# Optimization experiments

Measured on AMD Instinct MI355X. Metric: run time of the kernel, lower is better.

The kernel has to match this reference:

```python
import jax, jax.numpy as jnp
import numpy as np
import functools, math

HEADS = 16


def _query_chunk_attention(query, key, value, precision, key_chunk_size=4096):
    # query: (q_chunk, bh, d); key/value: (kv, bh, d)
    num_kv, num_heads, k_features = key.shape[-3:]
    v_features = value.shape[-1]
    key_chunk_size = min(key_chunk_size, num_kv)
    query = query / jnp.sqrt(k_features)

    @functools.partial(jax.checkpoint, prevent_cse=False)
    def summarize_chunk(query, key, value):
        attn_weights = jnp.einsum("...qhd,...khd->...qhk", query, key, precision=precision)
        max_score = jnp.max(attn_weights, axis=-1, keepdims=True)
        max_score = jax.lax.stop_gradient(max_score)
        exp_weights = jnp.exp(attn_weights - max_score)
        exp_values = jnp.einsum("...vhf,...qhv->...qhf", value, exp_weights, precision=precision)
        max_score = jnp.einsum("...qhk->...qh", max_score)
        return exp_values, exp_weights.sum(axis=-1), max_score

    def chunk_scanner(chunk_idx):
        key_chunk = jax.lax.dynamic_slice(
            key, [chunk_idx, 0, 0], [key_chunk_size, num_heads, k_features])
        value_chunk = jax.lax.dynamic_slice(
            value, [chunk_idx, 0, 0], [key_chunk_size, num_heads, v_features])
        return summarize_chunk(query, key_chunk, value_chunk)

    chunk_values, chunk_weights, chunk_max = jax.lax.map(
        chunk_scanner, xs=jnp.arange(0, num_kv, key_chunk_size))
    # online softmax rescaling across kv chunks
    global_max = jnp.max(chunk_max, axis=0, keepdims=True)
    max_diffs = jnp.exp(chunk_max - global_max)
    chunk_values = chunk_values * jnp.expand_dims(max_diffs, axis=-1)
    chunk_weights = chunk_weights * max_diffs
    all_values = chunk_values.sum(axis=0)
    all_weights = jnp.expand_dims(chunk_weights, -1).sum(axis=0)
    return all_values / all_weights


def jax_memory_efficient_attention(query, key, value,
                                   precision=jax.lax.Precision.HIGHEST,
                                   query_chunk_size=1024, key_chunk_size=4096):
    # query: (q_len, bh, d)
    num_q, num_heads, q_features = query.shape[-3:]

    def chunk_scanner(chunk_idx, _):
        query_chunk = jax.lax.dynamic_slice(
            query, [chunk_idx, 0, 0],
            [min(query_chunk_size, num_q), num_heads, q_features])
        return (chunk_idx + query_chunk_size,
                _query_chunk_attention(query_chunk, key, value, precision, key_chunk_size))

    _, res = jax.lax.scan(chunk_scanner, 0, xs=None,
                          length=math.ceil(num_q / query_chunk_size))
    return jnp.concatenate(res, axis=-3)


def _reshape_heads_to_batch_dim(tensor, heads):
    b, s, d = tensor.shape
    t = tensor.reshape(b, s, heads, d // heads).transpose(0, 2, 1, 3)
    return t.reshape(b * heads, s, d // heads)


def _attention_fwd(query, key, value):
    heads = HEADS
    q = _reshape_heads_to_batch_dim(query, heads).transpose(1, 0, 2)  # (s, b*h, dh)
    k = _reshape_heads_to_batch_dim(key, heads).transpose(1, 0, 2)
    v = _reshape_heads_to_batch_dim(value, heads).transpose(1, 0, 2)
    flatten_latent_dim = q.shape[-3]
    if flatten_latent_dim % 64 == 0:
        query_chunk_size = flatten_latent_dim // 64
    elif flatten_latent_dim % 16 == 0:
        query_chunk_size = flatten_latent_dim // 16
    elif flatten_latent_dim % 4 == 0:
        query_chunk_size = flatten_latent_dim // 4
    else:
        query_chunk_size = flatten_latent_dim
    out = jax_memory_efficient_attention(q, k, v,
                                         query_chunk_size=query_chunk_size,
                                         key_chunk_size=4096 * 4)
    return out.transpose(1, 0, 2)  # (b*h, s, dh)


def setup_inputs() -> dict:
    key = jax.random.key(0)
    k1, k2, k3 = jax.random.split(key, 3)
    B, S, D = 2, 4096, 1024
    return {
        "query": jax.random.normal(k1, (B, S, D), dtype=jnp.float32),
        "key": jax.random.normal(k2, (B, S, D), dtype=jnp.float32),
        "value": jax.random.normal(k3, (B, S, D), dtype=jnp.float32),
    }


def reference(query, key, value):
    return _attention_fwd(query, key, value)
```

## Files before the change

### kernel.cpp

```cpp
#include <hip/hip_runtime.h>
#include <math.h>

#define SEQ    4096
#define DH     64
#define DMODEL 1024
#define NBH    32
#define NT64   64
#define LOG2E  1.44269504088896340736f

typedef __attribute__((ext_vector_type(8)))  short short8;
typedef __attribute__((ext_vector_type(4)))  float f32x4;
typedef __attribute__((ext_vector_type(16))) float f32x16;
typedef __attribute__((ext_vector_type(2)))  unsigned uint2v;

#define WS_KV_BYTES   33554432ull
#define WS_NEED_SPLIT 68157440ull

__device__ __forceinline__ unsigned short f2bf(float f) {
  union { float f; unsigned u; } x; x.f = f;
  unsigned r = x.u + 0x7FFFu + ((x.u >> 16) & 1u);
  return (unsigned short)(r >> 16);
}
__device__ __forceinline__ float bf2f(unsigned short u) {
  union { unsigned u; float f; } x; x.u = ((unsigned)u) << 16;
  return x.f;
}
__device__ __forceinline__ unsigned cvtpk_bf16(float lo, float hi) {
  unsigned r;
  asm("v_cvt_pk_bf16_f32 %0, %1, %2" : "=v"(r) : "v"(lo), "v"(hi));
  return r;
}

__global__ __launch_bounds__(256)
void prep(const float* __restrict__ Kp, const float* __restrict__ Vp,
          unsigned short* __restrict__ ws) {
  __shared__ unsigned short Kt[128 * DH];
  __shared__ unsigned short Vt[128 * DH];
  const int blk = blockIdx.x;
  const int bh = blk >> 5, t128 = blk & 31;
  const int b = bh >> 4, h = bh & 15;
  const size_t gbase = (size_t)b * SEQ * DMODEL + (size_t)h * DH +
                       (size_t)t128 * 128 * DMODEL;
  const float* Kb = Kp + gbase;
  const float* Vb = Vp + gbase;
  unsigned short* wt = ws + (size_t)bh * NT64 * 8192 + (size_t)(2 * t128) * 8192;
  const int tid = threadIdx.x;

#pragma unroll
  for (int c = 0; c < 8; ++c) {
    const int idx = c * 256 + tid;
    const int row = idx >> 4, dc = idx & 15;
    f32x4 kf = *(const f32x4*)(Kb + (size_t)row * DMODEL + dc * 4);
    f32x4 vf = *(const f32x4*)(Vb + (size_t)row * DMODEL + dc * 4);
    uint2v ku, vu;
    ku[0] = (unsigned)f2bf(kf[0]) | ((unsigned)f2bf(kf[1]) << 16);
    ku[1] = (unsigned)f2bf(kf[2]) | ((unsigned)f2bf(kf[3]) << 16);
    vu[0] = (unsigned)f2bf(vf[0]) | ((unsigned)f2bf(vf[1]) << 16);
    vu[1] = (unsigned)f2bf(vf[2]) | ((unsigned)f2bf(vf[3]) << 16);
    *(uint2v*)&Kt[row * 64 + dc * 4] = ku;
    *(uint2v*)&Vt[row * 64 + dc * 4] = vu;
  }
  __syncthreads();

#pragma unroll
  for (int c = 0; c < 4; ++c) {
    const int idx = c * 256 + tid;
    const int l31 = idx & 31, hi = (idx >> 5) & 1, d4 = (idx >> 6) & 3, kb = idx >> 8;
    const int tau = kb >> 1, kb2 = kb & 1;
    short8 v = *(const short8*)&Kt[(kb * 32 + l31) * 64 + d4 * 16 + hi * 8];
    *(short8*)&wt[tau * 8192 + (((kb2 * 4 + d4) * 2 + hi) * 32 + l31) * 8] = v;
  }
#pragma unroll
  for (int c = 0; c < 4; ++c) {
    const int idx = c * 256 + tid;
    const int l31 = idx & 31, dt = (idx >> 5) & 1, hi = (idx >> 6) & 1, k16 = idx >> 7;
    const int tau = k16 >> 2, k162 = k16 & 3;
    const int d = dt * 32 + l31, kb0 = k16 * 16 + hi * 8;
    short8 v;
#pragma unroll
    for (int j = 0; j < 8; ++j) v[j] = (short)Vt[(kb0 + j) * 64 + d];
    *(short8*)&wt[tau * 8192 + 4096 + (((k162 * 2 + hi) * 64) + dt * 32 + l31) * 8] = v;
  }
}

template <bool SPLIT>
__global__ __launch_bounds__(256, 2)
void fattn(const float* __restrict__ Qp,
           const unsigned short* __restrict__ ws,
           float* __restrict__ Op) {
  __shared__ __align__(16) char lds[2][16384];

  const int tid  = threadIdx.x;
  const int lane = tid & 63;
  const int w    = tid >> 6;
  const int hi   = lane >> 5;
  const int l31  = lane & 31;

  int bh, qt, sh, rid;
  if (SPLIT) {
    const int id = blockIdx.x;
    rid = (id & 7) * 128 + (id >> 3);
    bh = rid >> 5; qt = (rid >> 1) & 15; sh = rid & 1;
  } else {
    const int id = blockIdx.x;
    rid = (id & 7) * 64 + (id >> 3);
    bh = rid >> 4; qt = rid & 15; sh = 0;
  }
  const int NTloc = SPLIT ? 32 : 64;
  const int t0    = sh * 32;
  const int q0    = qt * 256 + w * 64;

  const int b = bh >> 4, h = bh & 15;
  const float* Qb = Qp + (size_t)b * SEQ * DMODEL + (size_t)h * DH;
  const char* wsb = (const char*)(ws + (size_t)bh * NT64 * 8192);

  short8 qb[2][4];
#pragma unroll
  for (int s = 0; s < 2; ++s) {
    const float* qr = Qb + (size_t)(q0 + s * 32 + l31) * DMODEL;
    const float sc = 0.125f * LOG2E;
#pragma unroll
    for (int d4 = 0; d4 < 4; ++d4) {
      const float* p = qr + d4 * 16 + hi * 8;
      f32x4 f0 = *(const f32x4*)p;
      f32x4 f1 = *(const f32x4*)(p + 4);
      short8 v;
#pragma unroll
      for (int i = 0; i < 4; ++i) {
        v[i]     = (short)f2bf(f0[i] * sc);
        v[i + 4] = (short)f2bf(f1[i] * sc);
      }
      qb[s][d4] = v;
    }
  }

  f32x16 ZERO;
#pragma unroll
  for (int r = 0; r < 16; ++r) ZERO[r] = 0.f;
  f32x16 acc[2][2];
#pragma unroll
  for (int s = 0; s < 2; ++s)
#pragma unroll
    for (int dt = 0; dt < 2; ++dt) acc[s][dt] = ZERO;
  float lsum[2] = {0.f, 0.f};

  const int laneK = hi * 512 + l31 * 16;
  const int laneV = hi * 1024 + l31 * 16;

#define STAGE(buf_, tau_)                                                     \
  {                                                                           \
    const char* src_ = wsb + (size_t)(tau_) * 16384;                          \
    char* dst_ = &lds[buf_][0];                                               \
    _Pragma("unroll")                                                         \
    for (int c_ = 0; c_ < 4; ++c_) {                                          \
      __builtin_amdgcn_global_load_lds(                                       \
          (const __attribute__((address_space(1))) void*)(src_ + c_ * 4096 +  \
                                                          tid * 16),          \
          (__attribute__((address_space(3))) void*)(dst_ + c_ * 4096 +        \
                                                    tid * 16),                \
          16, 0, 0);                                                          \
    }                                                                         \
  }

  STAGE(0, t0);
  __syncthreads();

  for (int t = 0; t < NTloc; ++t) {
    const int buf = t & 1;
    if (t + 1 < NTloc) STAGE(buf ^ 1, t0 + t + 1);
    const char* Lk = &lds[buf][0];
    const char* Lv = &lds[buf][8192];

#pragma unroll
    for (int kb = 0; kb < 2; ++kb) {
      short8 ka[4];
#pragma unroll
      for (int d4 = 0; d4 < 4; ++d4)
        ka[d4] = *(const short8*)(Lk + kb * 4096 + d4 * 1024 + laneK);
      f32x16 zA, zB;
      __builtin_amdgcn_s_setprio(1);
      zA = __builtin_amdgcn_mfma_f32_32x32x16_bf16(ka[0], qb[0][0], ZERO, 0, 0, 0);
      zB = __builtin_amdgcn_mfma_f32_32x32x16_bf16(ka[0], qb[1][0], ZERO, 0, 0, 0);
      zA = __builtin_amdgcn_mfma_f32_32x32x16_bf16(ka[1], qb[0][1], zA, 0, 0, 0);
      zB = __builtin_amdgcn_mfma_f32_32x32x16_bf16(ka[1], qb[1][1], zB, 0, 0, 0);
      zA = __builtin_amdgcn_mfma_f32_32x32x16_bf16(ka[2], qb[0][2], zA, 0, 0, 0);
      zB = __builtin_amdgcn_mfma_f32_32x32x16_bf16(ka[2], qb[1][2], zB, 0, 0, 0);
      zA = __builtin_amdgcn_mfma_f32_32x32x16_bf16(ka[3], qb[0][3], zA, 0, 0, 0);
      zB = __builtin_amdgcn_mfma_f32_32x32x16_bf16(ka[3], qb[1][3], zB, 0, 0, 0);
      __builtin_amdgcn_s_setprio(0);

#pragma unroll
      for (int r = 0; r < 16; ++r) zA[r] = __builtin_amdgcn_exp2f(zA[r]);
#pragma unroll
      for (int r = 0; r < 16; ++r) zB[r] = __builtin_amdgcn_exp2f(zB[r]);
      {
        float a0 = (zA[0] + zA[1]) + (zA[2] + zA[3]);
        float a1 = (zA[4] + zA[5]) + (zA[6] + zA[7]);
        float a2 = (zA[8] + zA[9]) + (zA[10] + zA[11]);
        float a3 = (zA[12] + zA[13]) + (zA[14] + zA[15]);
        lsum[0] += (a0 + a1) + (a2 + a3);
        float b0 = (zB[0] + zB[1]) + (zB[2] + zB[3]);
        float b1 = (zB[4] + zB[5]) + (zB[6] + zB[7]);
        float b2 = (zB[8] + zB[9]) + (zB[10] + zB[11]);
        float b3 = (zB[12] + zB[13]) + (zB[14] + zB[15]);
        lsum[1] += (b0 + b1) + (b2 + b3);
      }

#pragma unroll
      for (int s = 0; s < 2; ++s) {
        const int R = 8 * s;
        unsigned a0 = cvtpk_bf16(zA[R + 0], zA[R + 1]);
        unsigned c0 = cvtpk_bf16(zA[R + 4], zA[R + 5]);
        unsigned a1 = cvtpk_bf16(zA[R + 2], zA[R + 3]);
        unsigned c1 = cvtpk_bf16(zA[R + 6], zA[R + 7]);
        asm("v_permlane32_swap_b32 %0, %1" : "+v"(a0), "+v"(c0));
        asm("v_permlane32_swap_b32 %0, %1" : "+v"(a1), "+v"(c1));
        union { unsigned u[4]; short8 s8; } pwA;
        pwA.u[0] = a0; pwA.u[1] = a1; pwA.u[2] = c0; pwA.u[3] = c1;
        unsigned d0 = cvtpk_bf16(zB[R + 0], zB[R + 1]);
        unsigned e0 = cvtpk_bf16(zB[R + 4], zB[R + 5]);
        unsigned d1 = cvtpk_bf16(zB[R + 2], zB[R + 3]);
        unsigned e1 = cvtpk_bf16(zB[R + 6], zB[R + 7]);
        asm("v_permlane32_swap_b32 %0, %1" : "+v"(d0), "+v"(e0));
        asm("v_permlane32_swap_b32 %0, %1" : "+v"(d1), "+v"(e1));
        union { unsigned u[4]; short8 s8; } pwB;
        pwB.u[0] = d0; pwB.u[1] = d1; pwB.u[2] = e0; pwB.u[3] = e1;

        const int k16 = kb * 2 + s;
        short8 vb0 = *(const short8*)(Lv + k16 * 2048 + laneV);
        short8 vb1 = *(const short8*)(Lv + k16 * 2048 + 512 + laneV);
        __builtin_amdgcn_s_setprio(1);
        acc[0][0] = __builtin_amdgcn_mfma_f32_32x32x16_bf16(pwA.s8, vb0, acc[0][0], 0, 0, 0);
        acc[0][1] = __builtin_amdgcn_mfma_f32_32x32x16_bf16(pwA.s8, vb1, acc[0][1], 0, 0, 0);
        acc[1][0] = __builtin_amdgcn_mfma_f32_32x32x16_bf16(pwB.s8, vb0, acc[1][0], 0, 0, 0);
        acc[1][1] = __builtin_amdgcn_mfma_f32_32x32x16_bf16(pwB.s8, vb1, acc[1][1], 0, 0, 0);
        __builtin_amdgcn_s_setprio(0);
      }
    }
    __syncthreads();
  }

  if (SPLIT) {
    unsigned short* part = (unsigned short*)((char*)nullptr);
    part = (unsigned short*)((const char*)ws + WS_KV_BYTES) + (size_t)rid * 16384;
    float* lout = (float*)((const char*)ws + WS_KV_BYTES + WS_KV_BYTES) + (size_t)rid * 256;
#pragma unroll
    for (int s = 0; s < 2; ++s) {
      const float lt = lsum[s] + __shfl_xor(lsum[s], 32, 64);
      if (hi == 0) lout[w * 64 + s * 32 + l31] = lt;
#pragma unroll
      for (int dt = 0; dt < 2; ++dt)
#pragma unroll
        for (int r = 0; r < 16; ++r) {
          const int qrow = (r & 3) + 8 * (r >> 2) + 4 * hi;
          part[(w * 64 + s * 32 + qrow) * 64 + dt * 32 + l31] = f2bf(acc[s][dt][r]);
        }
    }
  } else {
#pragma unroll
    for (int s = 0; s < 2; ++s) {
      const float lt  = lsum[s] + __shfl_xor(lsum[s], 32, 64);
      const float inv = 1.0f / lt;
#pragma unroll
      for (int dt = 0; dt < 2; ++dt)
#pragma unroll
        for (int r = 0; r < 16; ++r) {
          const int qrow = (r & 3) + 8 * (r >> 2) + 4 * hi;
          const float iv = __shfl(inv, qrow + (lane & 32), 64);
          const size_t row = (size_t)bh * SEQ + q0 + s * 32 + qrow;
          Op[row * DH + dt * 32 + l31] = acc[s][dt][r] * iv;
        }
    }
  }
}

__global__ __launch_bounds__(256)
void combine(const unsigned short* __restrict__ ws, float* __restrict__ Op) {
  const unsigned short* part = (const unsigned short*)((const char*)ws + WS_KV_BYTES);
  const float* lsum = (const float*)((const char*)ws + 2 * WS_KV_BYTES);
  const int gid = blockIdx.x * 256 + threadIdx.x;
  const int bq = gid >> 11;
  const int rem = gid & 2047;
  const int q = rem >> 3, dc = rem & 7;
  const int pid0 = bq * 2, pid1 = pid0 + 1;
  short8 A0 = *(const short8*)&part[(size_t)pid0 * 16384 + q * 64 + dc * 8];
  short8 A1 = *(const short8*)&part[(size_t)pid1 * 16384 + q * 64 + dc * 8];
  const float l = lsum[pid0 * 256 + q] + lsum[pid1 * 256 + q];
  const float inv = 1.0f / l;
  const int bh = bq >> 4, qt = bq & 15;
  float* o = Op + ((size_t)bh * SEQ + qt * 256 + q) * DH + dc * 8;
  f32x4 o0, o1;
#pragma unroll
  for (int j = 0; j < 4; ++j) {
    o0[j] = (bf2f((unsigned short)A0[j]) + bf2f((unsigned short)A1[j])) * inv;
    o1[j] = (bf2f((unsigned short)A0[j + 4]) + bf2f((unsigned short)A1[j + 4])) * inv;
  }
  *(f32x4*)o = o0;
  *(f32x4*)(o + 4) = o1;
}

extern "C" void kernel_launch(void* const* d_in, const int* in_sizes, int n_in,
                              void* d_out, int out_size, void* d_ws, size_t ws_size,
                              hipStream_t stream) {
  const float* Q = (const float*)d_in[0];
  const float* K = (const float*)d_in[1];
  const float* V = (const float*)d_in[2];
  float* O = (float*)d_out;
  unsigned short* ws = (unsigned short*)d_ws;

  prep<<<dim3(NBH * 32), dim3(256), 0, stream>>>(K, V, ws);
  if (ws_size >= WS_NEED_SPLIT) {
    fattn<true><<<dim3(1024), dim3(256), 0, stream>>>(Q, ws, O);
    combine<<<dim3(4096), dim3(256), 0, stream>>>(ws, O);
  } else {
    fattn<false><<<dim3(512), dim3(256), 0, stream>>>(Q, ws, O);
  }
}
```

Baseline: 165.4 us.

## Halve per-warp query rows and software-pipeline QK with softmax/PV across K blocks

Each warp now handles 32 query rows instead of 64, so the grid doubles and launch bounds allow three blocks per CU, cutting register pressure and raising occupancy. The main loop is restructured into a ping-pong pipeline: the QK MFMA for one 32-key half-block is issued while the exp/convert/PV work of the previous half-block runs, with the next-tile stage moved between two barriers. The intent is to overlap MFMA with the exp/VALU work and hide latency. In exchange, K/V tiles are reloaded from global memory twice as often per query, and there is an extra barrier per tile.

New measurement: 170.3 us. 1.03x slower.

```diff
diff --git a/kernel.cpp b/kernel.cpp
--- a/kernel.cpp
+++ b/kernel.cpp
@@ -83,8 +83,57 @@
   }
 }
 
+__device__ __forceinline__ f32x16 qk_block(const char* Lk, int kbpar, int laneK,
+                                           const short8* qb, const f32x16& ZERO) {
+  short8 ka0 = *(const short8*)(Lk + kbpar * 4096 + 0 * 1024 + laneK);
+  short8 ka1 = *(const short8*)(Lk + kbpar * 4096 + 1 * 1024 + laneK);
+  short8 ka2 = *(const short8*)(Lk + kbpar * 4096 + 2 * 1024 + laneK);
+  short8 ka3 = *(const short8*)(Lk + kbpar * 4096 + 3 * 1024 + laneK);
+  f32x16 z;
+  __builtin_amdgcn_s_setprio(1);
+  z = __builtin_amdgcn_mfma_f32_32x32x16_bf16(ka0, qb[0], ZERO, 0, 0, 0);
+  z = __builtin_amdgcn_mfma_f32_32x32x16_bf16(ka1, qb[1], z, 0, 0, 0);
+  z = __builtin_amdgcn_mfma_f32_32x32x16_bf16(ka2, qb[2], z, 0, 0, 0);
+  z = __builtin_amdgcn_mfma_f32_32x32x16_bf16(ka3, qb[3], z, 0, 0, 0);
+  __builtin_amdgcn_s_setprio(0);
+  return z;
+}
+
+__device__ __forceinline__ void proc_block(f32x16& z, const char* Lv, int k16base,
+                                           int laneV, f32x16& accL, f32x16& accH,
+                                           float& lsum) {
+#pragma unroll
+  for (int r = 0; r < 16; ++r) z[r] = __builtin_amdgcn_exp2f(z[r]);
+  {
+    float s0 = (z[0] + z[1]) + (z[2] + z[3]);
+    float s1 = (z[4] + z[5]) + (z[6] + z[7]);
+    float s2 = (z[8] + z[9]) + (z[10] + z[11]);
+    float s3 = (z[12] + z[13]) + (z[14] + z[15]);
+    lsum += (s0 + s1) + (s2 + s3);
+  }
+#pragma unroll
+  for (int s = 0; s < 2; ++s) {
+    const int R = 8 * s;
+    unsigned a0 = cvtpk_bf16(z[R + 0], z[R + 1]);
+    unsigned c0 = cvtpk_bf16(z[R + 4], z[R + 5]);
+    unsigned a1 = cvtpk_bf16(z[R + 2], z[R + 3]);
+    unsigned c1 = cvtpk_bf16(z[R + 6], z[R + 7]);
+    asm("v_permlane32_swap_b32 %0, %1" : "+v"(a0), "+v"(c0));
+    asm("v_permlane32_swap_b32 %0, %1" : "+v"(a1), "+v"(c1));
+    union { unsigned u[4]; short8 s8; } pw;
+    pw.u[0] = a0; pw.u[1] = a1; pw.u[2] = c0; pw.u[3] = c1;
+    const int k16 = k16base + s;
+    short8 vb0 = *(const short8*)(Lv + k16 * 2048 + laneV);
+    short8 vb1 = *(const short8*)(Lv + k16 * 2048 + 512 + laneV);
+    __builtin_amdgcn_s_setprio(1);
+    accL = __builtin_amdgcn_mfma_f32_32x32x16_bf16(pw.s8, vb0, accL, 0, 0, 0);
+    accH = __builtin_amdgcn_mfma_f32_32x32x16_bf16(pw.s8, vb1, accH, 0, 0, 0);
+    __builtin_amdgcn_s_setprio(0);
+  }
+}
+
 template <bool SPLIT>
-__global__ __launch_bounds__(256, 2)
+__global__ __launch_bounds__(256, 3)
 void fattn(const float* __restrict__ Qp,
            const unsigned short* __restrict__ ws,
            float* __restrict__ Op) {
@@ -96,28 +145,27 @@
   const int hi   = lane >> 5;
   const int l31  = lane & 31;
 
-  int bh, qt, sh, rid;
+  int bh, qc, sh, rid;
   if (SPLIT) {
     const int id = blockIdx.x;
-    rid = (id & 7) * 128 + (id >> 3);
-    bh = rid >> 5; qt = (rid >> 1) & 15; sh = rid & 1;
+    rid = (id & 7) * 256 + (id >> 3);
+    bh = rid >> 6; qc = (rid >> 1) & 31; sh = rid & 1;
   } else {
     const int id = blockIdx.x;
-    rid = (id & 7) * 64 + (id >> 3);
-    bh = rid >> 4; qt = rid & 15; sh = 0;
+    rid = (id & 7) * 128 + (id >> 3);
+    bh = rid >> 5; qc = rid & 31; sh = 0;
   }
   const int NTloc = SPLIT ? 32 : 64;
   const int t0    = sh * 32;
-  const int q0    = qt * 256 + w * 64;
+  const int q0    = qc * 128 + w * 32;
 
   const int b = bh >> 4, h = bh & 15;
   const float* Qb = Qp + (size_t)b * SEQ * DMODEL + (size_t)h * DH;
   const char* wsb = (const char*)(ws + (size_t)bh * NT64 * 8192);
 
-  short8 qb[2][4];
-#pragma unroll
-  for (int s = 0; s < 2; ++s) {
-    const float* qr = Qb + (size_t)(q0 + s * 32 + l31) * DMODEL;
+  short8 qb[4];
+  {
+    const float* qr = Qb + (size_t)(q0 + l31) * DMODEL;
     const float sc = 0.125f * LOG2E;
 #pragma unroll
     for (int d4 = 0; d4 < 4; ++d4) {
@@ -130,19 +178,15 @@
         v[i]     = (short)f2bf(f0[i] * sc);
         v[i + 4] = (short)f2bf(f1[i] * sc);
       }
-      qb[s][d4] = v;
+      qb[d4] = v;
     }
   }
 
   f32x16 ZERO;
 #pragma unroll
   for (int r = 0; r < 16; ++r) ZERO[r] = 0.f;
-  f32x16 acc[2][2];
-#pragma unroll
-  for (int s = 0; s < 2; ++s)
-#pragma unroll
-    for (int dt = 0; dt < 2; ++dt) acc[s][dt] = ZERO;
-  float lsum[2] = {0.f, 0.f};
+  f32x16 accL = ZERO, accH = ZERO;
+  float lsum = 0.f;
 
   const int laneK = hi * 512 + l31 * 16;
   const int laneV = hi * 1024 + l31 * 16;
@@ -165,113 +209,51 @@
   STAGE(0, t0);
   __syncthreads();
 
+  f32x16 zE, zO;
   for (int t = 0; t < NTloc; ++t) {
-    const int buf = t & 1;
-    if (t + 1 < NTloc) STAGE(buf ^ 1, t0 + t + 1);
-    const char* Lk = &lds[buf][0];
-    const char* Lv = &lds[buf][8192];
-
-#pragma unroll
-    for (int kb = 0; kb < 2; ++kb) {
-      short8 ka[4];
-#pragma unroll
-      for (int d4 = 0; d4 < 4; ++d4)
-        ka[d4] = *(const short8*)(Lk + kb * 4096 + d4 * 1024 + laneK);
-      f32x16 zA, zB;
-      __builtin_amdgcn_s_setprio(1);
-      zA = __builtin_amdgcn_mfma_f32_32x32x16_bf16(ka[0], qb[0][0], ZERO, 0, 0, 0);
-      zB = __builtin_amdgcn_mfma_f32_32x32x16_bf16(ka[0], qb[1][0], ZERO, 0, 0, 0);
-      zA = __builtin_amdgcn_mfma_f32_32x32x16_bf16(ka[1], qb[0][1], zA, 0, 0, 0);
-      zB = __builtin_amdgcn_mfma_f32_32x32x16_bf16(ka[1], qb[1][1], zB, 0, 0, 0);
-      zA = __builtin_amdgcn_mfma_f32_32x32x16_bf16(ka[2], qb[0][2], zA, 0, 0, 0);
-      zB = __builtin_amdgcn_mfma_f32_32x32x16_bf16(ka[2], qb[1][2], zB, 0, 0, 0);
-      zA = __builtin_amdgcn_mfma_f32_32x32x16_bf16(ka[3], qb[0][3], zA, 0, 0, 0);
-      zB = __builtin_amdgcn_mfma_f32_32x32x16_bf16(ka[3], qb[1][3], zB, 0, 0, 0);
-      __builtin_amdgcn_s_setprio(0);
-
-#pragma unroll
-      for (int r = 0; r < 16; ++r) zA[r] = __builtin_amdgcn_exp2f(zA[r]);
-#pragma unroll
-      for (int r = 0; r < 16; ++r) zB[r] = __builtin_amdgcn_exp2f(zB[r]);
-      {
-        float a0 = (zA[0] + zA[1]) + (zA[2] + zA[3]);
-        float a1 = (zA[4] + zA[5]) + (zA[6] + zA[7]);
-        float a2 = (zA[8] + zA[9]) + (zA[10] + zA[11]);
-        float a3 = (zA[12] + zA[13]) + (zA[14] + zA[15]);
-        lsum[0] += (a0 + a1) + (a2 + a3);
-        float b0 = (zB[0] + zB[1]) + (zB[2] + zB[3]);
-        float b1 = (zB[4] + zB[5]) + (zB[6] + zB[7]);
-        float b2 = (zB[8] + zB[9]) + (zB[10] + zB[11]);
-        float b3 = (zB[12] + zB[13]) + (zB[14] + zB[15]);
-        lsum[1] += (b0 + b1) + (b2 + b3);
-      }
-
-#pragma unroll
-      for (int s = 0; s < 2; ++s) {
-        const int R = 8 * s;
-        unsigned a0 = cvtpk_bf16(zA[R + 0], zA[R + 1]);
-        unsigned c0 = cvtpk_bf16(zA[R + 4], zA[R + 5]);
-        unsigned a1 = cvtpk_bf16(zA[R + 2], zA[R + 3]);
-        unsigned c1 = cvtpk_bf16(zA[R + 6], zA[R + 7]);
-        asm("v_permlane32_swap_b32 %0, %1" : "+v"(a0), "+v"(c0));
-        asm("v_permlane32_swap_b32 %0, %1" : "+v"(a1), "+v"(c1));
-        union { unsigned u[4]; short8 s8; } pwA;
-        pwA.u[0] = a0; pwA.u[1] = a1; pwA.u[2] = c0; pwA.u[3] = c1;
-        unsigned d0 = cvtpk_bf16(zB[R + 0], zB[R + 1]);
-        unsigned e0 = cvtpk_bf16(zB[R + 4], zB[R + 5]);
-        unsigned d1 = cvtpk_bf16(zB[R + 2], zB[R + 3]);
-        unsigned e1 = cvtpk_bf16(zB[R + 6], zB[R + 7]);
-        asm("v_permlane32_swap_b32 %0, %1" : "+v"(d0), "+v"(e0));
-        asm("v_permlane32_swap_b32 %0, %1" : "+v"(d1), "+v"(e1));
-        union { unsigned u[4]; short8 s8; } pwB;
-        pwB.u[0] = d0; pwB.u[1] = d1; pwB.u[2] = e0; pwB.u[3] = e1;
-
-        const int k16 = kb * 2 + s;
-        short8 vb0 = *(const short8*)(Lv + k16 * 2048 + laneV);
-        short8 vb1 = *(const short8*)(Lv + k16 * 2048 + 512 + laneV);
-        __builtin_amdgcn_s_setprio(1);
-        acc[0][0] = __builtin_amdgcn_mfma_f32_32x32x16_bf16(pwA.s8, vb0, acc[0][0], 0, 0, 0);
-        acc[0][1] = __builtin_amdgcn_mfma_f32_32x32x16_bf16(pwA.s8, vb1, acc[0][1], 0, 0, 0);
-        acc[1][0] = __builtin_amdgcn_mfma_f32_32x32x16_bf16(pwB.s8, vb0, acc[1][0], 0, 0, 0);
-        acc[1][1] = __builtin_amdgcn_mfma_f32_32x32x16_bf16(pwB.s8, vb1, acc[1][1], 0, 0, 0);
-        __builtin_amdgcn_s_setprio(0);
-      }
-    }
+    const int cur = t & 1;
+    const char* Lk  = &lds[cur][0];
+    const char* Lv  = &lds[cur][8192];
+    const char* LvO = &lds[cur ^ 1][8192];
+
+    zE = qk_block(Lk, 0, laneK, qb, ZERO);
+    if (t > 0)
+      proc_block(zO, LvO, 2, laneV, accL, accH, lsum);
     __syncthreads();
-  }
+    if (t + 1 < NTloc) STAGE(cur ^ 1, t0 + t + 1);
+    zO = qk_block(Lk, 1, laneK, qb, ZERO);
+    proc_block(zE, Lv, 0, laneV, accL, accH, lsum);
+    __syncthreads();
+  }
+  proc_block(zO, &lds[(NTloc - 1) & 1][8192], 2, laneV, accL, accH, lsum);
 
   if (SPLIT) {
-    unsigned short* part = (unsigned short*)((char*)nullptr);
-    part = (unsigned short*)((const char*)ws + WS_KV_BYTES) + (size_t)rid * 16384;
-    float* lout = (float*)((const char*)ws + WS_KV_BYTES + WS_KV_BYTES) + (size_t)rid * 256;
-#pragma unroll
-    for (int s = 0; s < 2; ++s) {
-      const float lt = lsum[s] + __shfl_xor(lsum[s], 32, 64);
-      if (hi == 0) lout[w * 64 + s * 32 + l31] = lt;
-#pragma unroll
-      for (int dt = 0; dt < 2; ++dt)
-#pragma unroll
-        for (int r = 0; r < 16; ++r) {
-          const int qrow = (r & 3) + 8 * (r >> 2) + 4 * hi;
-          part[(w * 64 + s * 32 + qrow) * 64 + dt * 32 + l31] = f2bf(acc[s][dt][r]);
-        }
+    unsigned short* part =
+        (unsigned short*)((char*)(unsigned short*)const_cast<unsigned short*>(ws) +
+                          WS_KV_BYTES) + (size_t)rid * 8192;
+    float* lout = (float*)((char*)const_cast<unsigned short*>(ws) +
+                           2 * WS_KV_BYTES) + (size_t)rid * 128;
+    const float lt = lsum + __shfl_xor(lsum, 32, 64);
+    if (hi == 0) lout[w * 32 + l31] = lt;
+#pragma unroll
+    for (int r = 0; r < 16; ++r) {
+      const int qrow = (r & 3) + 8 * (r >> 2) + 4 * hi;
+      part[(w * 32 + qrow) * 64 + l31]      = f2bf(accL[r]);
+      part[(w * 32 + qrow) * 64 + 32 + l31] = f2bf(accH[r]);
     }
   } else {
-#pragma unroll
-    for (int s = 0; s < 2; ++s) {
-      const float lt  = lsum[s] + __shfl_xor(lsum[s], 32, 64);
-      const float inv = 1.0f / lt;
-#pragma unroll
-      for (int dt = 0; dt < 2; ++dt)
-#pragma unroll
-        for (int r = 0; r < 16; ++r) {
-          const int qrow = (r & 3) + 8 * (r >> 2) + 4 * hi;
-          const float iv = __shfl(inv, qrow + (lane & 32), 64);
-          const size_t row = (size_t)bh * SEQ + q0 + s * 32 + qrow;
-          Op[row * DH + dt * 32 + l31] = acc[s][dt][r] * iv;
-        }
+    const float lt  = lsum + __shfl_xor(lsum, 32, 64);
+    const float inv = 1.0f / lt;
+#pragma unroll
+    for (int r = 0; r < 16; ++r) {
+      const int qrow = (r & 3) + 8 * (r >> 2) + 4 * hi;
+      const float iv = __shfl(inv, qrow + (lane & 32), 64);
+      const size_t row = (size_t)bh * SEQ + q0 + qrow;
+      Op[row * DH + l31]      = accL[r] * iv;
+      Op[row * DH + 32 + l31] = accH[r] * iv;
     }
   }
+#undef STAGE
 }
 
 __global__ __launch_bounds__(256)
@@ -279,16 +261,16 @@
   const unsigned short* part = (const unsigned short*)((const char*)ws + WS_KV_BYTES);
   const float* lsum = (const float*)((const char*)ws + 2 * WS_KV_BYTES);
   const int gid = blockIdx.x * 256 + threadIdx.x;
-  const int bq = gid >> 11;
-  const int rem = gid & 2047;
+  const int bqc = gid >> 10;
+  const int rem = gid & 1023;
   const int q = rem >> 3, dc = rem & 7;
-  const int pid0 = bq * 2, pid1 = pid0 + 1;
-  short8 A0 = *(const short8*)&part[(size_t)pid0 * 16384 + q * 64 + dc * 8];
-  short8 A1 = *(const short8*)&part[(size_t)pid1 * 16384 + q * 64 + dc * 8];
-  const float l = lsum[pid0 * 256 + q] + lsum[pid1 * 256 + q];
+  const int pid0 = bqc * 2, pid1 = pid0 + 1;
+  short8 A0 = *(const short8*)&part[(size_t)pid0 * 8192 + q * 64 + dc * 8];
+  short8 A1 = *(const short8*)&part[(size_t)pid1 * 8192 + q * 64 + dc * 8];
+  const float l = lsum[pid0 * 128 + q] + lsum[pid1 * 128 + q];
   const float inv = 1.0f / l;
-  const int bh = bq >> 4, qt = bq & 15;
-  float* o = Op + ((size_t)bh * SEQ + qt * 256 + q) * DH + dc * 8;
+  const int bh = bqc >> 5, qc = bqc & 31;
+  float* o = Op + ((size_t)bh * SEQ + qc * 128 + q) * DH + dc * 8;
   f32x4 o0, o1;
 #pragma unroll
   for (int j = 0; j < 4; ++j) {
@@ -310,9 +292,9 @@
 
   prep<<<dim3(NBH * 32), dim3(256), 0, stream>>>(K, V, ws);
   if (ws_size >= WS_NEED_SPLIT) {
-    fattn<true><<<dim3(1024), dim3(256), 0, stream>>>(Q, ws, O);
+    fattn<true><<<dim3(2048), dim3(256), 0, stream>>>(Q, ws, O);
     combine<<<dim3(4096), dim3(256), 0, stream>>>(ws, O);
   } else {
-    fattn<false><<<dim3(512), dim3(256), 0, stream>>>(Q, ws, O);
-  }
-}
+    fattn<false><<<dim3(1024), dim3(256), 0, stream>>>(Q, ws, O);
+  }
+}
```
